# Kernel tuning notes

Hardware: AMD Instinct MI355X
Metric: run time of the kernel (lower is better)

## Reference

```python
import jax, jax.numpy as jnp
import numpy as np

B, N, D_MODEL, H = 8, 1024, 768, 12
HD = D_MODEL // H  # head dim = 64
SCALE = D_MODEL ** (-0.5)  # NOTE: original scales by input_dim**-0.5, not head_dim**-0.5


def setup_inputs() -> dict:
    key = jax.random.key(0)
    k1, k2 = jax.random.split(key)
    x = jax.random.normal(k1, (B, N, D_MODEL), dtype=jnp.float32)
    # torch Linear weight is [out,in]; we store transposed [in,out] for x @ W
    w_qkv = jax.random.normal(k2, (D_MODEL, 3 * D_MODEL), dtype=jnp.float32) * (D_MODEL ** -0.5)
    b_qkv = jnp.zeros((3 * D_MODEL,), dtype=jnp.float32)
    return {"x": x, "w_qkv": w_qkv, "b_qkv": b_qkv}


def reference(x, w_qkv, b_qkv):
    # QKV projection: [B, N, 3*D]
    y = jnp.einsum("bnd,de->bne", x, w_qkv) + b_qkv
    # Faithful to einops 'b n (h d qkv) -> qkv b h n d': qkv is fastest-varying
    y = y.reshape(B, N, H, HD, 3)
    q = jnp.transpose(y[..., 0], (0, 2, 1, 3))  # [B, H, N, HD]
    k = jnp.transpose(y[..., 1], (0, 2, 1, 3))
    v = jnp.transpose(y[..., 2], (0, 2, 1, 3))
    energy = jnp.einsum("bhqd,bhkd->bhqk", q, k)
    attn = jax.nn.softmax(energy * SCALE, axis=-1)  # dropout is identity at eval
    out = jnp.einsum("bhqk,bhkd->bhqd", attn, v)
    # 'b h n d -> b n (h d)'
    return jnp.transpose(out, (0, 2, 1, 3)).reshape(B, N, D_MODEL)
```

## Files before the change

### kernel.cpp

```cpp
#include <hip/hip_runtime.h>
#include <hip/hip_bf16.h>
#include <stdint.h>

#define NB 8
#define NS 1024
#define DM 768
#define NH 12
#define DH 64
#define NE 2304
#define MTOT (NB*NS)

typedef unsigned short u16;
typedef __attribute__((ext_vector_type(8))) __bf16 bf16x8;
typedef __attribute__((ext_vector_type(4))) float floatx4;
typedef __attribute__((ext_vector_type(4))) uint32_t uint32x4;

#define WS_XB  0ull
#define WS_WT  12582912ull
#define WS_BR  16121856ull
#define WS_QB  16131072ull
#define WS_KB  28713984ull
#define WS_VT  41296896ull

#define QSC 0.05206490030275093f

__device__ __forceinline__ u16 f2bf(float f) {
  union { float f; uint32_t u; } v; v.f = f;
  uint32_t r = (v.u + 0x7fffu + ((v.u >> 16) & 1u)) >> 16;
  return (u16)r;
}

__device__ __forceinline__ void gload16(const void* g, void* l) {
  __builtin_amdgcn_global_load_lds(
      (const __attribute__((address_space(1))) void*)g,
      (__attribute__((address_space(3))) void*)l, 16, 0, 0);
}

__global__ void conv_x_kernel(const float4* __restrict__ x, u16* __restrict__ xb, int n4) {
  int i = blockIdx.x * blockDim.x + threadIdx.x;
  int stride = gridDim.x * blockDim.x;
  for (; i < n4; i += stride) {
    float4 v = x[i];
    ushort4 r;
    r.x = f2bf(v.x); r.y = f2bf(v.y); r.z = f2bf(v.z); r.w = f2bf(v.w);
    ((ushort4*)xb)[i] = r;
  }
}

__global__ void prep_bias_kernel(const float* __restrict__ b, float* __restrict__ br) {
  const int o = blockIdx.x * 256 + threadIdx.x;
  if (o < 3 * DM) {
    const int c = o / DM, n = o % DM;
    const int h = n >> 6, d = n & 63;
    float v = b[h * 192 + d * 3 + c];
    if (c == 0) v *= QSC;
    br[o] = v;
  }
}

__global__ void transpose_w_kernel(const float* __restrict__ w, u16* __restrict__ wt) {
  __shared__ float tile[32][33];
  const int e0 = blockIdx.x * 32, k0 = blockIdx.y * 32;
  const int tx = threadIdx.x, ty = threadIdx.y;
#pragma unroll
  for (int i = 0; i < 4; i++)
    tile[ty + i*8][tx] = w[(size_t)(k0 + ty + i*8) * NE + e0 + tx];
  __syncthreads();
#pragma unroll
  for (int i = 0; i < 4; i++) {
    const int e = e0 + ty + i*8;
    const int c = e % 3, h = e / 192, d = (e % 192) / 3;
    const float sc = (c == 0) ? QSC : 1.0f;
    wt[((size_t)c * DM + h*64 + d) * DM + k0 + tx] = f2bf(tile[tx][ty + i*8] * sc);
  }
}

__global__ __launch_bounds__(256) void qkv_gemm_kernel(
    const u16* __restrict__ xb, const u16* __restrict__ wt,
    const float* __restrict__ br,
    u16* __restrict__ qb, u16* __restrict__ kb, u16* __restrict__ vtb) {
  __shared__ __align__(16) u16 a_lds[2][128 * 32];
  __shared__ __align__(16) u16 b_lds[2][128 * 32];
  const int t  = threadIdx.x;
  const int w  = t >> 6, l = t & 63;
  const int wr = w >> 1, wc = w & 1;
  const int lq = l & 15, lg = l >> 4;
  const int m0  = (int)blockIdx.x * 128;
  const int n0  = (int)blockIdx.y * 128;
  const int cls = (int)blockIdx.z;

  floatx4 z = {0.f, 0.f, 0.f, 0.f};
  floatx4 acc[4][4];
#pragma unroll
  for (int i = 0; i < 4; i++)
#pragma unroll
    for (int j = 0; j < 4; j++) acc[i][j] = z;

  const int srow = t >> 2;
  const int scb  = (t & 3) ^ ((t >> 3) & 3);
  const u16* ga = xb + (size_t)m0 * DM + scb * 8;
  const u16* gb = wt + ((size_t)cls * DM + n0) * DM + scb * 8;
  const int rswz = (lq >> 1) & 3;

#define STAGE(buf, k0)                                                            \
  {                                                                               \
    _Pragma("unroll")                                                             \
    for (int i = 0; i < 2; i++) {                                                 \
      gload16(ga + (size_t)(i*64 + srow) * DM + (k0), (char*)a_lds[buf] + i*4096 + w*1024); \
      gload16(gb + (size_t)(i*64 + srow) * DM + (k0), (char*)b_lds[buf] + i*4096 + w*1024); \
    }                                                                             \
  }

#define COMPUTE(buf)                                                              \
  {                                                                               \
    bf16x8 af[4], bfr[4];                                                         \
    _Pragma("unroll")                                                             \
    for (int i = 0; i < 4; i++)                                                   \
      af[i] = *(const bf16x8*)((const char*)a_lds[buf] + (wr*64 + i*16 + lq)*64 + ((lg ^ rswz) * 16)); \
    _Pragma("unroll")                                                             \
    for (int j = 0; j < 4; j++)                                                   \
      bfr[j] = *(const bf16x8*)((const char*)b_lds[buf] + (wc*64 + j*16 + lq)*64 + ((lg ^ rswz) * 16)); \
    if (cls == 2) {                                                               \
      _Pragma("unroll")                                                           \
      for (int i = 0; i < 4; i++)                                                 \
        _Pragma("unroll")                                                         \
        for (int j = 0; j < 4; j++)                                               \
          acc[i][j] = __builtin_amdgcn_mfma_f32_16x16x32_bf16(bfr[j], af[i], acc[i][j], 0, 0, 0); \
    } else {                                                                      \
      _Pragma("unroll")                                                           \
      for (int i = 0; i < 4; i++)                                                 \
        _Pragma("unroll")                                                         \
        for (int j = 0; j < 4; j++)                                               \
          acc[i][j] = __builtin_amdgcn_mfma_f32_16x16x32_bf16(af[i], bfr[j], acc[i][j], 0, 0, 0); \
    }                                                                             \
  }

  STAGE(0, 0);
  __syncthreads();
  int cur = 0;
  for (int k0 = 32; k0 < DM; k0 += 32) {
    STAGE(cur ^ 1, k0);
    COMPUTE(cur);
    __syncthreads();
    cur ^= 1;
  }
  COMPUTE(cur);
#undef STAGE
#undef COMPUTE

  if (cls != 2) {
    u16* dst = (cls == 0) ? qb : kb;
#pragma unroll
    for (int j = 0; j < 4; j++) {
      const int n  = n0 + wc*64 + j*16 + lq;
      const int h  = n >> 6, d = n & 63;
      const float bv = br[cls * DM + n];
#pragma unroll
      for (int i = 0; i < 4; i++) {
        const int mb = m0 + wr*64 + i*16 + lg*4;
#pragma unroll
        for (int r = 0; r < 4; r++) {
          const int m = mb + r;
          const int bb = m >> 10, nn = m & 1023;
          dst[(((size_t)(bb * NH + h)) * NS + nn) * DH + d] = f2bf(acc[i][j][r] + bv);
        }
      }
    }
  } else {
    const int hq = (n0 + wc*64) >> 6;
#pragma unroll
    for (int j = 0; j < 4; j++) {
      float bvv[4];
#pragma unroll
      for (int r = 0; r < 4; r++)
        bvv[r] = br[2 * DM + n0 + wc*64 + j*16 + lg*4 + r];
#pragma unroll
      for (int i = 0; i < 4; i++) {
        const int m = m0 + wr*64 + i*16 + lq;
        const int bb = m >> 10, nn = m & 1023;
#pragma unroll
        for (int r = 0; r < 4; r++) {
          const int d = (j*16 + lg*4 + r) & 63;
          vtb[(((size_t)(bb * NH + hq)) * DH + d) * NS + nn] = f2bf(acc[i][j][r] + bvv[r]);
        }
      }
    }
  }
}

__global__ __launch_bounds__(256) void attn_kernel(
    const u16* __restrict__ qb, const u16* __restrict__ kb,
    const u16* __restrict__ vtb, float* __restrict__ out) {
  __shared__ __align__(16) u16 k_lds[64 * 64];
  __shared__ __align__(16) u16 v_lds[64 * 64];

  const int t = threadIdx.x, w = t >> 6, l = t & 63;
  const int bh = blockIdx.x >> 3, qblk = blockIdx.x & 7;
  const int bb = bh / NH, h = bh % NH;
  const int q0 = qblk * 128 + w * 32;
  const int lq = l & 15, lg = l >> 4;

  bf16x8 qf[2][2];
#pragma unroll
  for (int qt = 0; qt < 2; qt++) {
    const u16* qrow = qb + ((size_t)bh * NS + q0 + qt*16 + lq) * DH;
#pragma unroll
    for (int ds = 0; ds < 2; ds++)
      qf[qt][ds] = *(const bf16x8*)&qrow[lg*8 + ds*32];
  }

  float m2[2]    = {4.0f, 4.0f};
  float lsumP[2] = {0.f, 0.f};
  floatx4 z = {0.f, 0.f, 0.f, 0.f};
  floatx4 o[2][4];
#pragma unroll
  for (int qt = 0; qt < 2; qt++)
#pragma unroll
    for (int dt = 0; dt < 4; dt++) o[qt][dt] = z;

  const int srow = t >> 3;
  const int scb  = (t & 7) ^ (srow & 7);

  for (int kt0 = 0; kt0 < 16; kt0++) {
    const int k0 = kt0 * 64;
    __syncthreads();
#pragma unroll
    for (int i = 0; i < 2; i++) {
      const int row = i*32 + srow;
      gload16(kb  + ((size_t)bh * NS + k0 + row) * DH + scb*8, (char*)k_lds + i*4096 + w*1024);
      gload16(vtb + ((size_t)bh * DH + row) * NS + k0 + scb*8, (char*)v_lds + i*4096 + w*1024);
    }
    __syncthreads();

#pragma unroll
    for (int half = 0; half < 2; half++) {
      bf16x8 kf[2][2];
#pragma unroll
      for (int kt = 0; kt < 2; kt++) {
        const int krow = half*32 + ((lq >> 2) << 3) + kt*4 + (lq & 3);
#pragma unroll
        for (int ds = 0; ds < 2; ds++)
          kf[kt][ds] = *(const bf16x8*)((const char*)k_lds + krow*128 + ((ds*4 + lg) ^ (krow & 7))*16);
      }
      bf16x8 vf[4];
#pragma unroll
      for (int dt = 0; dt < 4; dt++) {
        const int vrow = dt*16 + lq;
        vf[dt] = *(const bf16x8*)((const char*)v_lds + vrow*128 + ((half*4 + lg) ^ (vrow & 7))*16);
      }

#pragma unroll
      for (int qt = 0; qt < 2; qt++) {
        floatx4 st0 = z, st1 = z;
        st0 = __builtin_amdgcn_mfma_f32_16x16x32_bf16(kf[0][0], qf[qt][0], st0, 0, 0, 0);
        st0 = __builtin_amdgcn_mfma_f32_16x16x32_bf16(kf[0][1], qf[qt][1], st0, 0, 0, 0);
        st1 = __builtin_amdgcn_mfma_f32_16x16x32_bf16(kf[1][0], qf[qt][0], st1, 0, 0, 0);
        st1 = __builtin_amdgcn_mfma_f32_16x16x32_bf16(kf[1][1], qf[qt][1], st1, 0, 0, 0);

        float p[8];
#pragma unroll
        for (int r = 0; r < 4; r++) { p[r] = st0[r]; p[4 + r] = st1[r]; }
        const float pmax = fmaxf(fmaxf(fmaxf(p[0], p[1]), fmaxf(p[2], p[3])),
                                 fmaxf(fmaxf(p[4], p[5]), fmaxf(p[6], p[7])));

        if (!__all(pmax - m2[qt] <= 8.0f)) {
          float mt = pmax;
          mt = fmaxf(mt, __shfl_xor(mt, 16));
          mt = fmaxf(mt, __shfl_xor(mt, 32));
          const float mnew = fmaxf(m2[qt], mt);
          const float corr = exp2f(m2[qt] - mnew);
          lsumP[qt] *= corr;
          float cr[4];
#pragma unroll
          for (int r = 0; r < 4; r++) cr[r] = __shfl(corr, lg*4 + r);
#pragma unroll
          for (int dt = 0; dt < 4; dt++)
#pragma unroll
            for (int r = 0; r < 4; r++) o[qt][dt][r] *= cr[r];
          m2[qt] = mnew;
        }

        const float m = m2[qt];
        float ls = 0.f;
        u16 pb[8];
#pragma unroll
        for (int e = 0; e < 8; e++) {
          const float pe = exp2f(p[e] - m);
          ls += pe;
          pb[e] = f2bf(pe);
        }
        lsumP[qt] += ls;

        uint32x4 pw;
        pw.x = (uint32_t)pb[0] | ((uint32_t)pb[1] << 16);
        pw.y = (uint32_t)pb[2] | ((uint32_t)pb[3] << 16);
        pw.z = (uint32_t)pb[4] | ((uint32_t)pb[5] << 16);
        pw.w = (uint32_t)pb[6] | ((uint32_t)pb[7] << 16);
        const bf16x8 pa = __builtin_bit_cast(bf16x8, pw);

#pragma unroll
        for (int dt = 0; dt < 4; dt++)
          o[qt][dt] = __builtin_amdgcn_mfma_f32_16x16x32_bf16(pa, vf[dt], o[qt][dt], 0, 0, 0);
      }
    }
  }

#pragma unroll
  for (int qt = 0; qt < 2; qt++) {
    float ls = lsumP[qt];
    ls += __shfl_xor(ls, 16);
    ls += __shfl_xor(ls, 32);
    const float inv = 1.0f / ls;
    float ir[4];
#pragma unroll
    for (int r = 0; r < 4; r++) ir[r] = __shfl(inv, lg*4 + r);
#pragma unroll
    for (int dt = 0; dt < 4; dt++)
#pragma unroll
      for (int r = 0; r < 4; r++) {
        const int n = q0 + qt*16 + lg*4 + r;
        out[((size_t)bb * NS + n) * DM + h*DH + dt*16 + lq] = o[qt][dt][r] * ir[r];
      }
  }
}

extern "C" void kernel_launch(void* const* d_in, const int* in_sizes, int n_in,
                              void* d_out, int out_size, void* d_ws, size_t ws_size,
                              hipStream_t stream) {
  const float* x     = (const float*)d_in[0];
  const float* w_qkv = (const float*)d_in[1];
  const float* b_qkv = (const float*)d_in[2];
  float* out = (float*)d_out;
  char* ws = (char*)d_ws;

  u16* xb   = (u16*)(ws + WS_XB);
  u16* wt   = (u16*)(ws + WS_WT);
  float* br = (float*)(ws + WS_BR);
  u16* qb   = (u16*)(ws + WS_QB);
  u16* kb   = (u16*)(ws + WS_KB);
  u16* vtb  = (u16*)(ws + WS_VT);

  conv_x_kernel<<<1024, 256, 0, stream>>>((const float4*)x, xb, MTOT * DM / 4);
  prep_bias_kernel<<<9, 256, 0, stream>>>(b_qkv, br);
  transpose_w_kernel<<<dim3(NE/32, DM/32), dim3(32, 8), 0, stream>>>(w_qkv, wt);
  qkv_gemm_kernel<<<dim3(MTOT/128, DM/128, 3), 256, 0, stream>>>(xb, wt, br, qb, kb, vtb);
  attn_kernel<<<(NB*NH) * (NS/128), 256, 0, stream>>>(qb, kb, vtb, out);
}
```

Measured before the change: 147.5 us.

## Restructure QKV GEMM as single-wave 64x64 blocks with XCD-aware grid mapping

New measurement: 133.3 us. 1.11x faster.

```diff
diff --git a/kernel.cpp b/kernel.cpp
--- a/kernel.cpp
+++ b/kernel.cpp
@@ -75,19 +75,24 @@
   }
 }
 
-__global__ __launch_bounds__(256) void qkv_gemm_kernel(
+__global__ __launch_bounds__(64, 4) void qkv_gemm_kernel(
     const u16* __restrict__ xb, const u16* __restrict__ wt,
     const float* __restrict__ br,
     u16* __restrict__ qb, u16* __restrict__ kb, u16* __restrict__ vtb) {
-  __shared__ __align__(16) u16 a_lds[2][128 * 32];
-  __shared__ __align__(16) u16 b_lds[2][128 * 32];
+  __shared__ __align__(16) u16 a_lds[2][64 * 32];
+  __shared__ __align__(16) u16 b_lds[2][64 * 32];
   const int t  = threadIdx.x;
-  const int w  = t >> 6, l = t & 63;
-  const int wr = w >> 1, wc = w & 1;
-  const int lq = l & 15, lg = l >> 4;
-  const int m0  = (int)blockIdx.x * 128;
-  const int n0  = (int)blockIdx.y * 128;
-  const int cls = (int)blockIdx.z;
+  const int lq = t & 15, lg = t >> 4;
+
+  const int bid    = (int)blockIdx.x;
+  const int xcd    = bid & 7;
+  const int within = bid >> 3;
+  const int mi     = within & 15;
+  const int ni     = within >> 4;
+  const int m0     = (xcd * 16 + mi) * 64;
+  const int cls    = ni / 12;
+  const int nb     = ni % 12;
+  const int n0     = nb * 64;
 
   floatx4 z = {0.f, 0.f, 0.f, 0.f};
   floatx4 acc[4][4];
@@ -105,9 +110,9 @@
 #define STAGE(buf, k0)                                                            \
   {                                                                               \
     _Pragma("unroll")                                                             \
-    for (int i = 0; i < 2; i++) {                                                 \
-      gload16(ga + (size_t)(i*64 + srow) * DM + (k0), (char*)a_lds[buf] + i*4096 + w*1024); \
-      gload16(gb + (size_t)(i*64 + srow) * DM + (k0), (char*)b_lds[buf] + i*4096 + w*1024); \
+    for (int i = 0; i < 4; i++) {                                                 \
+      gload16(ga + (size_t)(i*16 + srow) * DM + (k0), (char*)a_lds[buf] + i*1024); \
+      gload16(gb + (size_t)(i*16 + srow) * DM + (k0), (char*)b_lds[buf] + i*1024); \
     }                                                                             \
   }
 
@@ -116,10 +121,10 @@
     bf16x8 af[4], bfr[4];                                                         \
     _Pragma("unroll")                                                             \
     for (int i = 0; i < 4; i++)                                                   \
-      af[i] = *(const bf16x8*)((const char*)a_lds[buf] + (wr*64 + i*16 + lq)*64 + ((lg ^ rswz) * 16)); \
+      af[i] = *(const bf16x8*)((const char*)a_lds[buf] + (i*16 + lq)*64 + ((lg ^ rswz) * 16)); \
     _Pragma("unroll")                                                             \
     for (int j = 0; j < 4; j++)                                                   \
-      bfr[j] = *(const bf16x8*)((const char*)b_lds[buf] + (wc*64 + j*16 + lq)*64 + ((lg ^ rswz) * 16)); \
+      bfr[j] = *(const bf16x8*)((const char*)b_lds[buf] + (j*16 + lq)*64 + ((lg ^ rswz) * 16)); \
     if (cls == 2) {                                                               \
       _Pragma("unroll")                                                           \
       for (int i = 0; i < 4; i++)                                                 \
@@ -136,14 +141,15 @@
   }
 
   STAGE(0, 0);
-  __syncthreads();
   int cur = 0;
-  for (int k0 = 32; k0 < DM; k0 += 32) {
-    STAGE(cur ^ 1, k0);
+  for (int kt = 0; kt < 23; ++kt) {
+    asm volatile("s_waitcnt lgkmcnt(0)" ::: "memory");
+    STAGE(cur ^ 1, 32 * (kt + 1));
+    asm volatile("s_waitcnt vmcnt(8)" ::: "memory");
     COMPUTE(cur);
-    __syncthreads();
     cur ^= 1;
   }
+  asm volatile("s_waitcnt vmcnt(0)" ::: "memory");
   COMPUTE(cur);
 #undef STAGE
 #undef COMPUTE
@@ -152,36 +158,34 @@
     u16* dst = (cls == 0) ? qb : kb;
 #pragma unroll
     for (int j = 0; j < 4; j++) {
-      const int n  = n0 + wc*64 + j*16 + lq;
-      const int h  = n >> 6, d = n & 63;
-      const float bv = br[cls * DM + n];
+      const int d  = j*16 + lq;
+      const float bv = br[cls * DM + n0 + d];
 #pragma unroll
       for (int i = 0; i < 4; i++) {
-        const int mb = m0 + wr*64 + i*16 + lg*4;
+        const int mb = m0 + i*16 + lg*4;
 #pragma unroll
         for (int r = 0; r < 4; r++) {
           const int m = mb + r;
           const int bb = m >> 10, nn = m & 1023;
-          dst[(((size_t)(bb * NH + h)) * NS + nn) * DH + d] = f2bf(acc[i][j][r] + bv);
+          dst[(((size_t)(bb * NH + nb)) * NS + nn) * DH + d] = f2bf(acc[i][j][r] + bv);
         }
       }
     }
   } else {
-    const int hq = (n0 + wc*64) >> 6;
 #pragma unroll
     for (int j = 0; j < 4; j++) {
       float bvv[4];
 #pragma unroll
       for (int r = 0; r < 4; r++)
-        bvv[r] = br[2 * DM + n0 + wc*64 + j*16 + lg*4 + r];
+        bvv[r] = br[2 * DM + n0 + j*16 + lg*4 + r];
 #pragma unroll
       for (int i = 0; i < 4; i++) {
-        const int m = m0 + wr*64 + i*16 + lq;
+        const int m = m0 + i*16 + lq;
         const int bb = m >> 10, nn = m & 1023;
 #pragma unroll
         for (int r = 0; r < 4; r++) {
-          const int d = (j*16 + lg*4 + r) & 63;
-          vtb[(((size_t)(bb * NH + hq)) * DH + d) * NS + nn] = f2bf(acc[i][j][r] + bvv[r]);
+          const int d = j*16 + lg*4 + r;
+          vtb[(((size_t)(bb * NH + nb)) * DH + d) * NS + nn] = f2bf(acc[i][j][r] + bvv[r]);
         }
       }
     }
@@ -343,6 +347,6 @@
   conv_x_kernel<<<1024, 256, 0, stream>>>((const float4*)x, xb, MTOT * DM / 4);
   prep_bias_kernel<<<9, 256, 0, stream>>>(b_qkv, br);
   transpose_w_kernel<<<dim3(NE/32, DM/32), dim3(32, 8), 0, stream>>>(w_qkv, wt);
-  qkv_gemm_kernel<<<dim3(MTOT/128, DM/128, 3), 256, 0, stream>>>(xb, wt, br, qb, kb, vtb);
+  qkv_gemm_kernel<<<4608, 64, 0, stream>>>(xb, wt, br, qb, kb, vtb);
   attn_kernel<<<(NB*NH) * (NS/128), 256, 0, stream>>>(qb, kb, vtb, out);
 }
```
